# Kernel optimization log

Measured on AMD Instinct MI355X. Metric: run time of the kernel, lower is better.

Reference implementation:

```python
import jax, jax.numpy as jnp
import numpy as np

B, N, E, H = 8, 1024, 768, 12
HD = E // H  # head_dim = 64
EPS = 1e-5


def setup_inputs() -> dict:
    key = jax.random.key(0)
    ks = jax.random.split(key, 3)
    x = jax.random.normal(ks[0], (B, N, E), dtype=jnp.float32)
    # Packed in-projection like torch nn.MultiheadAttention (in_proj_weight [3E, E])
    w_qkv = jax.random.normal(ks[1], (3 * E, E), dtype=jnp.float32) * (1.0 / np.sqrt(E))
    b_qkv = jnp.zeros((3 * E,), dtype=jnp.float32)
    w_out = jax.random.normal(ks[2], (E, E), dtype=jnp.float32) * (1.0 / np.sqrt(E))
    b_out = jnp.zeros((E,), dtype=jnp.float32)
    ln_g = jnp.ones((E,), dtype=jnp.float32)
    ln_b = jnp.zeros((E,), dtype=jnp.float32)
    return {"x": x, "ln_g": ln_g, "ln_b": ln_b, "w_qkv": w_qkv,
            "b_qkv": b_qkv, "w_out": w_out, "b_out": b_out}


def reference(x, ln_g, ln_b, w_qkv, b_qkv, w_out, b_out):
    # LayerNorm over last dim (eps=1e-5, elementwise affine)
    mu = jnp.mean(x, axis=-1, keepdims=True)
    var = jnp.mean(jnp.square(x - mu), axis=-1, keepdims=True)
    xn = (x - mu) * jax.lax.rsqrt(var + EPS) * ln_g + ln_b

    # Packed QKV projection: torch does x @ in_proj_weight.T + in_proj_bias
    qkv = jnp.einsum('bne,fe->bnf', xn, w_qkv) + b_qkv  # [B, N, 3E]
    q, k, v = jnp.split(qkv, 3, axis=-1)
    # Split heads -> [B, H, N, HD]
    q = q.reshape(B, N, H, HD).transpose(0, 2, 1, 3)
    k = k.reshape(B, N, H, HD).transpose(0, 2, 1, 3)
    v = v.reshape(B, N, H, HD).transpose(0, 2, 1, 3)

    scale = 1.0 / np.sqrt(HD)
    scores = jnp.einsum('bhqd,bhkd->bhqk', q * scale, k)  # [B, H, N, N]
    attn = jax.nn.softmax(scores, axis=-1)
    # (attn_dropout=0.0; need_weights=True forces this manual path in torch,
    #  averaged weights attn.mean(axis=1) are computed but not returned here
    #  since return_attention_map defaults to False)
    ctx = jnp.einsum('bhqk,bhkd->bhqd', attn, v)  # [B, H, N, HD]
    ctx = ctx.transpose(0, 2, 1, 3).reshape(B, N, E)

    out = jnp.einsum('bne,fe->bnf', ctx, w_out) + b_out  # out_proj
    return out
```

## Files before the change

### kernel.cpp

```cpp
#include <hip/hip_runtime.h>
#include <hip/hip_bf16.h>
#include <stdint.h>

#define B_ 8
#define N_ 1024
#define E_ 768
#define H_ 12
#define HD_ 64
#define M_ (B_ * N_)

typedef __attribute__((ext_vector_type(8))) short bf8_t;
typedef __attribute__((ext_vector_type(4))) float f4_t;

__device__ __forceinline__ unsigned short f2bf(float f) {
  unsigned u = __builtin_bit_cast(unsigned, f);
  unsigned r = (u + 0x7fffu + ((u >> 16) & 1u)) >> 16;
  return (unsigned short)r;
}

__device__ __forceinline__ unsigned cvt_pk_bf16(float lo, float hi) {
  unsigned r;
  asm("v_cvt_pk_bf16_f32 %0, %1, %2" : "=v"(r) : "v"(lo), "v"(hi));
  return r;
}

__device__ __forceinline__ void load_lds16(const void* g, void* l) {
  __builtin_amdgcn_global_load_lds(
      (__attribute__((address_space(1))) void*)(g),
      (__attribute__((address_space(3))) void*)(l), 16, 0, 0);
}

__device__ __forceinline__ int swz(int row) {
  return ((row ^ (row >> 3)) & 7) << 3;
}

#define F3(a, b, c) fmaxf(fmaxf((a), (b)), (c))

__global__ void k_cast_bf16(const float* __restrict__ in,
                            unsigned short* __restrict__ out, int n4) {
  int i = blockIdx.x * blockDim.x + threadIdx.x;
  if (i < n4) {
    float4 v = ((const float4*)in)[i];
    ushort4 o;
    o.x = f2bf(v.x); o.y = f2bf(v.y); o.z = f2bf(v.z); o.w = f2bf(v.w);
    ((ushort4*)out)[i] = o;
  }
}

__global__ __launch_bounds__(192) void k_ln(const float* __restrict__ x,
                                            const float* __restrict__ g,
                                            const float* __restrict__ bta,
                                            unsigned short* __restrict__ xn) {
  int row = blockIdx.x;
  int t = threadIdx.x;
  float4 v = ((const float4*)(x + (size_t)row * E_))[t];
  float s = v.x + v.y + v.z + v.w;
  float s2 = v.x * v.x + v.y * v.y + v.z * v.z + v.w * v.w;
  for (int off = 32; off; off >>= 1) {
    s += __shfl_xor(s, off, 64);
    s2 += __shfl_xor(s2, off, 64);
  }
  __shared__ float red[6];
  int lane = t & 63, wv = t >> 6;
  if (lane == 0) { red[wv] = s; red[3 + wv] = s2; }
  __syncthreads();
  s = red[0] + red[1] + red[2];
  s2 = red[3] + red[4] + red[5];
  float mu = s * (1.0f / E_);
  float var = s2 * (1.0f / E_) - mu * mu;
  float rstd = rsqrtf(var + 1e-5f);
  float4 gg = ((const float4*)g)[t];
  float4 bb = ((const float4*)bta)[t];
  ushort4 o;
  o.x = f2bf((v.x - mu) * rstd * gg.x + bb.x);
  o.y = f2bf((v.y - mu) * rstd * gg.y + bb.y);
  o.z = f2bf((v.z - mu) * rstd * gg.z + bb.z);
  o.w = f2bf((v.w - mu) * rstd * gg.w + bb.w);
  ((ushort4*)(xn + (size_t)row * E_))[t] = o;
}

template <int EPI>
__global__ __launch_bounds__(256) void k_gemm_bt(
    const unsigned short* __restrict__ A,
    const unsigned short* __restrict__ W,
    const float* __restrict__ bias,
    unsigned short* __restrict__ oQ, unsigned short* __restrict__ oK,
    unsigned short* __restrict__ oVt, float* __restrict__ oF,
    int K, int Nf) {
  __shared__ unsigned short Al[2][128 * 64];
  __shared__ unsigned short Bl[2][128 * 64];
  const int nbx = Nf >> 7;
  const int nwg = nbx << 6;
  const int orig = blockIdx.y * nbx + blockIdx.x;
  const int id = (orig & 7) * (nwg >> 3) + (orig >> 3);
  const int n0 = (id % nbx) * 128, m0 = (id / nbx) * 128;
  const int tid = threadIdx.x;
  const int lane = tid & 63, wv = tid >> 6;
  const int wr = wv >> 1, wc = wv & 1;
  const int g = lane >> 4, l15 = lane & 15;
  f4_t acc[4][4] = {};

  auto stage = [&](int k0, int buf) {
#pragma unroll
    for (int i = 0; i < 4; ++i) {
      int e = (i * 256 + tid) * 8;
      int r = e >> 6;
      int c = (e & 63) ^ swz(r);
      load_lds16(A + (size_t)(m0 + r) * K + (k0 + c), &Al[buf][e]);
      load_lds16(W + (size_t)(n0 + r) * K + (k0 + c), &Bl[buf][e]);
    }
  };

  stage(0, 0);
  __syncthreads();
  int cur = 0;

  for (int k0 = 0; k0 < K; k0 += 64) {
    if (k0 + 64 < K) stage(k0 + 64, cur ^ 1);
    const unsigned short* Ac = Al[cur];
    const unsigned short* Bc = Bl[cur];
#pragma unroll
    for (int kk = 0; kk < 2; ++kk) {
      bf8_t af[4], bfr[4];
#pragma unroll
      for (int mi = 0; mi < 4; ++mi) {
        int ar = wr * 64 + mi * 16 + l15;
        af[mi] = *(const bf8_t*)&Ac[(ar * 64 + kk * 32 + g * 8) ^ swz(ar)];
      }
#pragma unroll
      for (int ni = 0; ni < 4; ++ni) {
        int br = wc * 64 + ni * 16 + l15;
        bfr[ni] = *(const bf8_t*)&Bc[(br * 64 + kk * 32 + g * 8) ^ swz(br)];
      }
#pragma unroll
      for (int mi = 0; mi < 4; ++mi)
#pragma unroll
        for (int ni = 0; ni < 4; ++ni)
          acc[mi][ni] = __builtin_amdgcn_mfma_f32_16x16x32_bf16(
              af[mi], bfr[ni], acc[mi][ni], 0, 0, 0);
    }
    __syncthreads();
    cur ^= 1;
  }

#pragma unroll
  for (int mi = 0; mi < 4; ++mi) {
#pragma unroll
    for (int ni = 0; ni < 4; ++ni) {
      int f = n0 + wc * 64 + ni * 16 + l15;
      float bs = bias[f];
#pragma unroll
      for (int i = 0; i < 4; ++i) {
        int m = m0 + wr * 64 + mi * 16 + g * 4 + i;
        float val = acc[mi][ni][i] + bs;
        if (EPI == 0) {
          int bb = m >> 10, n = m & 1023;
          int which = f / E_;
          int e2 = f - which * E_;
          int h = e2 >> 6, d = e2 & 63;
          size_t qk = (((size_t)bb * H_ + h) * N_ + n) * HD_ + d;
          if (which == 0) oQ[qk] = f2bf(val * 0.1803368801f);
          else if (which == 1) oK[qk] = f2bf(val);
          else oVt[(((size_t)bb * H_ + h) * HD_ + d) * N_ + n] = f2bf(val);
        } else {
          oF[(size_t)m * E_ + f] = val;
        }
      }
    }
  }
}

__global__ __launch_bounds__(256) void k_attn(
    const unsigned short* __restrict__ Q,
    const unsigned short* __restrict__ Kb,
    const unsigned short* __restrict__ Vt,
    unsigned short* __restrict__ ctx) {
  __shared__ unsigned short Kl[2][64 * 64];
  __shared__ unsigned short Vl[2][64 * 64];
  __shared__ unsigned short Pl[4][16 * 64];
  const int bh = blockIdx.x;
  const int qt = blockIdx.y;
  const int tid = threadIdx.x;
  const int lane = tid & 63, wv = tid >> 6;
  const int g = lane >> 4, l15 = lane & 15;

  const unsigned short* Qp = Q + ((size_t)bh * N_ + qt * 64 + wv * 16) * HD_;
  bf8_t qf[2];
#pragma unroll
  for (int kk = 0; kk < 2; ++kk)
    qf[kk] = *(const bf8_t*)&Qp[(size_t)l15 * HD_ + kk * 32 + g * 8];

  f4_t o[4] = {};
  float mrow = -1e30f, lrow = 0.f;
  const unsigned short* Kbase = Kb + (size_t)bh * N_ * HD_;
  const unsigned short* Vbase = Vt + (size_t)bh * HD_ * N_;

  auto stage = [&](int t, int buf) {
#pragma unroll
    for (int i = 0; i < 2; ++i) {
      int e = (i * 256 + tid) * 8;
      int r = e >> 6;
      int c = (e & 63) ^ swz(r);
      load_lds16(Kbase + (size_t)(t * 64 + r) * HD_ + c, &Kl[buf][e]);
      load_lds16(Vbase + (size_t)r * N_ + (t * 64 + c), &Vl[buf][e]);
    }
  };

  stage(0, 0);
  __syncthreads();
  int cur = 0;
  unsigned short* Pw = &Pl[wv][0];

  for (int t = 0; t < 16; ++t) {
    if (t + 1 < 16) stage(t + 1, cur ^ 1);
    const unsigned short* Klc = Kl[cur];
    const unsigned short* Vlc = Vl[cur];

    f4_t s[4] = {};
    __builtin_amdgcn_s_setprio(1);
#pragma unroll
    for (int ni = 0; ni < 4; ++ni) {
      int krow = ni * 16 + l15;
#pragma unroll
      for (int kk = 0; kk < 2; ++kk) {
        bf8_t kf = *(const bf8_t*)&Klc[(krow * 64 + kk * 32 + g * 8) ^ swz(krow)];
        s[ni] = __builtin_amdgcn_mfma_f32_16x16x32_bf16(kf, qf[kk], s[ni], 0, 0, 0);
      }
    }
    __builtin_amdgcn_s_setprio(0);

    float t0 = F3(s[0][0], s[0][1], s[0][2]);
    float t1 = F3(s[0][3], s[1][0], s[1][1]);
    float t2 = F3(s[1][2], s[1][3], s[2][0]);
    float t3 = F3(s[2][1], s[2][2], s[2][3]);
    float t4 = F3(s[3][0], s[3][1], s[3][2]);
    float mx = fmaxf(F3(F3(t0, t1, t2), t3, t4), s[3][3]);
    mx = fmaxf(mx, __shfl_xor(mx, 16, 64));
    mx = fmaxf(mx, __shfl_xor(mx, 32, 64));

    if (!__all(mx - mrow <= 8.0f)) {
      float mnew = fmaxf(mrow, mx);
      float al = exp2f(mrow - mnew);
      lrow *= al;
#pragma unroll
      for (int di = 0; di < 4; ++di)
#pragma unroll
        for (int i = 0; i < 4; ++i) o[di][i] *= al;
      mrow = mnew;
    }

    float r = 0.f;
#pragma unroll
    for (int ni = 0; ni < 4; ++ni)
#pragma unroll
      for (int i = 0; i < 4; ++i) {
        float p = exp2f(s[ni][i] - mrow);
        s[ni][i] = p;
        r += p;
      }
    r += __shfl_xor(r, 16, 64);
    r += __shfl_xor(r, 32, 64);
    lrow += r;

#pragma unroll
    for (int ni = 0; ni < 4; ++ni) {
      uint2 pk;
      pk.x = cvt_pk_bf16(s[ni][0], s[ni][1]);
      pk.y = cvt_pk_bf16(s[ni][2], s[ni][3]);
      int pe = l15 * 64 + ((ni * 16 + g * 4) ^ ((l15 & 7) << 3));
      *(uint2*)&Pw[pe] = pk;
    }
    asm volatile("s_waitcnt lgkmcnt(0)" ::: "memory");
    __builtin_amdgcn_sched_barrier(0);

    __builtin_amdgcn_s_setprio(1);
#pragma unroll
    for (int kk = 0; kk < 2; ++kk) {
      bf8_t pf = *(const bf8_t*)&Pw[l15 * 64 + (((kk * 32 + g * 8)) ^ ((l15 & 7) << 3))];
#pragma unroll
      for (int di = 0; di < 4; ++di) {
        int vrow = di * 16 + l15;
        bf8_t vf = *(const bf8_t*)&Vlc[(vrow * 64 + kk * 32 + g * 8) ^ swz(vrow)];
        o[di] = __builtin_amdgcn_mfma_f32_16x16x32_bf16(vf, pf, o[di], 0, 0, 0);
      }
    }
    __builtin_amdgcn_s_setprio(0);

    __syncthreads();
    cur ^= 1;
  }

  float rinv = 1.0f / lrow;
#pragma unroll
  for (int di = 0; di < 4; ++di) {
    uint2 pk;
    pk.x = cvt_pk_bf16(o[di][0] * rinv, o[di][1] * rinv);
    pk.y = cvt_pk_bf16(o[di][2] * rinv, o[di][3] * rinv);
    int oe = l15 * 64 + ((di * 16 + g * 4) ^ ((l15 & 7) << 3));
    *(uint2*)&Pw[oe] = pk;
  }
  asm volatile("s_waitcnt lgkmcnt(0)" ::: "memory");
  __builtin_amdgcn_sched_barrier(0);

  const int bb = bh / H_, h = bh - bb * H_;
  const int rr = lane >> 2, cb = (lane & 3) * 16;
#pragma unroll
  for (int m2 = 0; m2 < 2; ++m2) {
    int e = rr * 64 + ((cb + 8 * m2) ^ ((rr & 7) << 3));
    bf8_t val = *(const bf8_t*)&Pw[e];
    unsigned short* dst =
        ctx + ((size_t)bb * N_ + qt * 64 + wv * 16 + rr) * E_ + h * HD_ + cb + 8 * m2;
    *(bf8_t*)dst = val;
  }
}

extern "C" void kernel_launch(void* const* d_in, const int* in_sizes, int n_in,
                              void* d_out, int out_size, void* d_ws, size_t ws_size,
                              hipStream_t stream) {
  const float* x     = (const float*)d_in[0];
  const float* ln_g  = (const float*)d_in[1];
  const float* ln_b  = (const float*)d_in[2];
  const float* w_qkv = (const float*)d_in[3];
  const float* b_qkv = (const float*)d_in[4];
  const float* w_out = (const float*)d_in[5];
  const float* b_out = (const float*)d_in[6];
  float* out = (float*)d_out;

  char* ws = (char*)d_ws;
  const size_t SZ = (size_t)M_ * E_ * 2;
  unsigned short* xn    = (unsigned short*)(ws);
  unsigned short* qb    = (unsigned short*)(ws + SZ);
  unsigned short* kbuf  = (unsigned short*)(ws + 2 * SZ);
  unsigned short* vtb   = (unsigned short*)(ws + 3 * SZ);
  unsigned short* ctx   = (unsigned short*)(ws + 4 * SZ);
  unsigned short* wqkvb = (unsigned short*)(ws + 5 * SZ);
  unsigned short* woutb = (unsigned short*)(ws + 5 * SZ + (size_t)3 * E_ * E_ * 2);

  int n1 = 3 * E_ * E_ / 4;
  k_cast_bf16<<<(n1 + 255) / 256, 256, 0, stream>>>(w_qkv, wqkvb, n1);
  int n2 = E_ * E_ / 4;
  k_cast_bf16<<<(n2 + 255) / 256, 256, 0, stream>>>(w_out, woutb, n2);

  k_ln<<<M_, 192, 0, stream>>>(x, ln_g, ln_b, xn);

  k_gemm_bt<0><<<dim3(18, 64), 256, 0, stream>>>(xn, wqkvb, b_qkv, qb, kbuf, vtb,
                                                 nullptr, E_, 3 * E_);
  k_attn<<<dim3(96, 16), 256, 0, stream>>>(qb, kbuf, vtb, ctx);
  k_gemm_bt<1><<<dim3(6, 64), 256, 0, stream>>>(ctx, woutb, b_out, nullptr, nullptr,
                                                nullptr, out, E_, E_);
}
```

Before: 165.6 us.

## Process two query tiles per attention block to reuse K/V tiles

Each attention block now handles 128 query rows, with every wave holding two independent 16-row query fragments that share each staged K/V tile from LDS. The grid is halved along the query dimension, so K/V global traffic and staging per query row drop and MFMA work per LDS read doubles. The per-tile cross-lane row-sum shuffles are deferred to the end, and the max shuffles now run only when the rescale branch fires. This raises register and LDS use per block and halves the number of blocks (768), which may lower occupancy and load balance across CUs.

```diff
diff --git a/kernel.cpp b/kernel.cpp
--- a/kernel.cpp
+++ b/kernel.cpp
@@ -177,21 +177,24 @@
     unsigned short* __restrict__ ctx) {
   __shared__ unsigned short Kl[2][64 * 64];
   __shared__ unsigned short Vl[2][64 * 64];
-  __shared__ unsigned short Pl[4][16 * 64];
+  __shared__ unsigned short Pl[4][2][16 * 64];
   const int bh = blockIdx.x;
   const int qt = blockIdx.y;
   const int tid = threadIdx.x;
   const int lane = tid & 63, wv = tid >> 6;
   const int g = lane >> 4, l15 = lane & 15;
 
-  const unsigned short* Qp = Q + ((size_t)bh * N_ + qt * 64 + wv * 16) * HD_;
-  bf8_t qf[2];
-#pragma unroll
-  for (int kk = 0; kk < 2; ++kk)
-    qf[kk] = *(const bf8_t*)&Qp[(size_t)l15 * HD_ + kk * 32 + g * 8];
-
-  f4_t o[4] = {};
-  float mrow = -1e30f, lrow = 0.f;
+  const unsigned short* Qp = Q + ((size_t)bh * N_ + qt * 128 + wv * 16) * HD_;
+  bf8_t qfa[2], qfb[2];
+#pragma unroll
+  for (int kk = 0; kk < 2; ++kk) {
+    qfa[kk] = *(const bf8_t*)&Qp[(size_t)l15 * HD_ + kk * 32 + g * 8];
+    qfb[kk] = *(const bf8_t*)&Qp[(size_t)(64 + l15) * HD_ + kk * 32 + g * 8];
+  }
+
+  f4_t oa[4] = {}, ob[4] = {};
+  float mra = -1e30f, lra = 0.f;
+  float mrb = -1e30f, lrb = 0.f;
   const unsigned short* Kbase = Kb + (size_t)bh * N_ * HD_;
   const unsigned short* Vbase = Vt + (size_t)bh * HD_ * N_;
 
@@ -209,14 +212,15 @@
   stage(0, 0);
   __syncthreads();
   int cur = 0;
-  unsigned short* Pw = &Pl[wv][0];
+  unsigned short* Pwa = &Pl[wv][0][0];
+  unsigned short* Pwb = &Pl[wv][1][0];
 
   for (int t = 0; t < 16; ++t) {
     if (t + 1 < 16) stage(t + 1, cur ^ 1);
     const unsigned short* Klc = Kl[cur];
     const unsigned short* Vlc = Vl[cur];
 
-    f4_t s[4] = {};
+    f4_t sa[4] = {}, sb[4] = {};
     __builtin_amdgcn_s_setprio(1);
 #pragma unroll
     for (int ni = 0; ni < 4; ++ni) {
@@ -224,51 +228,63 @@
 #pragma unroll
       for (int kk = 0; kk < 2; ++kk) {
         bf8_t kf = *(const bf8_t*)&Klc[(krow * 64 + kk * 32 + g * 8) ^ swz(krow)];
-        s[ni] = __builtin_amdgcn_mfma_f32_16x16x32_bf16(kf, qf[kk], s[ni], 0, 0, 0);
+        sa[ni] = __builtin_amdgcn_mfma_f32_16x16x32_bf16(kf, qfa[kk], sa[ni], 0, 0, 0);
+        sb[ni] = __builtin_amdgcn_mfma_f32_16x16x32_bf16(kf, qfb[kk], sb[ni], 0, 0, 0);
       }
     }
     __builtin_amdgcn_s_setprio(0);
 
-    float t0 = F3(s[0][0], s[0][1], s[0][2]);
-    float t1 = F3(s[0][3], s[1][0], s[1][1]);
-    float t2 = F3(s[1][2], s[1][3], s[2][0]);
-    float t3 = F3(s[2][1], s[2][2], s[2][3]);
-    float t4 = F3(s[3][0], s[3][1], s[3][2]);
-    float mx = fmaxf(F3(F3(t0, t1, t2), t3, t4), s[3][3]);
-    mx = fmaxf(mx, __shfl_xor(mx, 16, 64));
-    mx = fmaxf(mx, __shfl_xor(mx, 32, 64));
-
-    if (!__all(mx - mrow <= 8.0f)) {
-      float mnew = fmaxf(mrow, mx);
-      float al = exp2f(mrow - mnew);
-      lrow *= al;
+    float ta0 = F3(sa[0][0], sa[0][1], sa[0][2]);
+    float ta1 = F3(sa[0][3], sa[1][0], sa[1][1]);
+    float ta2 = F3(sa[1][2], sa[1][3], sa[2][0]);
+    float ta3 = F3(sa[2][1], sa[2][2], sa[2][3]);
+    float ta4 = F3(sa[3][0], sa[3][1], sa[3][2]);
+    float mxa = fmaxf(F3(F3(ta0, ta1, ta2), ta3, ta4), sa[3][3]);
+    float tb0 = F3(sb[0][0], sb[0][1], sb[0][2]);
+    float tb1 = F3(sb[0][3], sb[1][0], sb[1][1]);
+    float tb2 = F3(sb[1][2], sb[1][3], sb[2][0]);
+    float tb3 = F3(sb[2][1], sb[2][2], sb[2][3]);
+    float tb4 = F3(sb[3][0], sb[3][1], sb[3][2]);
+    float mxb = fmaxf(F3(F3(tb0, tb1, tb2), tb3, tb4), sb[3][3]);
+
+    bool ok = (mxa - mra <= 8.0f) && (mxb - mrb <= 8.0f);
+    if (!__all(ok)) {
+      float Ma = fmaxf(mxa, __shfl_xor(mxa, 16, 64));
+      Ma = fmaxf(Ma, __shfl_xor(Ma, 32, 64));
+      float Mb = fmaxf(mxb, __shfl_xor(mxb, 16, 64));
+      Mb = fmaxf(Mb, __shfl_xor(Mb, 32, 64));
+      float mna = fmaxf(mra, Ma), mnb = fmaxf(mrb, Mb);
+      float ala = exp2f(mra - mna), alb = exp2f(mrb - mnb);
+      lra *= ala; lrb *= alb;
 #pragma unroll
       for (int di = 0; di < 4; ++di)
 #pragma unroll
-        for (int i = 0; i < 4; ++i) o[di][i] *= al;
-      mrow = mnew;
-    }
-
-    float r = 0.f;
+        for (int i = 0; i < 4; ++i) { oa[di][i] *= ala; ob[di][i] *= alb; }
+      mra = mna; mrb = mnb;
+    }
+
+    float ra = 0.f, rb = 0.f;
 #pragma unroll
     for (int ni = 0; ni < 4; ++ni)
 #pragma unroll
       for (int i = 0; i < 4; ++i) {
-        float p = exp2f(s[ni][i] - mrow);
-        s[ni][i] = p;
-        r += p;
-      }
-    r += __shfl_xor(r, 16, 64);
-    r += __shfl_xor(r, 32, 64);
-    lrow += r;
+        float pa = exp2f(sa[ni][i] - mra);
+        float pb = exp2f(sb[ni][i] - mrb);
+        sa[ni][i] = pa; sb[ni][i] = pb;
+        ra += pa; rb += pb;
+      }
+    lra += ra; lrb += rb;
 
 #pragma unroll
     for (int ni = 0; ni < 4; ++ni) {
-      uint2 pk;
-      pk.x = cvt_pk_bf16(s[ni][0], s[ni][1]);
-      pk.y = cvt_pk_bf16(s[ni][2], s[ni][3]);
       int pe = l15 * 64 + ((ni * 16 + g * 4) ^ ((l15 & 7) << 3));
-      *(uint2*)&Pw[pe] = pk;
+      uint2 pka, pkb;
+      pka.x = cvt_pk_bf16(sa[ni][0], sa[ni][1]);
+      pka.y = cvt_pk_bf16(sa[ni][2], sa[ni][3]);
+      pkb.x = cvt_pk_bf16(sb[ni][0], sb[ni][1]);
+      pkb.y = cvt_pk_bf16(sb[ni][2], sb[ni][3]);
+      *(uint2*)&Pwa[pe] = pka;
+      *(uint2*)&Pwb[pe] = pkb;
     }
     asm volatile("s_waitcnt lgkmcnt(0)" ::: "memory");
     __builtin_amdgcn_sched_barrier(0);
@@ -276,12 +292,15 @@
     __builtin_amdgcn_s_setprio(1);
 #pragma unroll
     for (int kk = 0; kk < 2; ++kk) {
-      bf8_t pf = *(const bf8_t*)&Pw[l15 * 64 + (((kk * 32 + g * 8)) ^ ((l15 & 7) << 3))];
+      int pe = l15 * 64 + ((kk * 32 + g * 8) ^ ((l15 & 7) << 3));
+      bf8_t pfa = *(const bf8_t*)&Pwa[pe];
+      bf8_t pfb = *(const bf8_t*)&Pwb[pe];
 #pragma unroll
       for (int di = 0; di < 4; ++di) {
         int vrow = di * 16 + l15;
         bf8_t vf = *(const bf8_t*)&Vlc[(vrow * 64 + kk * 32 + g * 8) ^ swz(vrow)];
-        o[di] = __builtin_amdgcn_mfma_f32_16x16x32_bf16(vf, pf, o[di], 0, 0, 0);
+        oa[di] = __builtin_amdgcn_mfma_f32_16x16x32_bf16(vf, pfa, oa[di], 0, 0, 0);
+        ob[di] = __builtin_amdgcn_mfma_f32_16x16x32_bf16(vf, pfb, ob[di], 0, 0, 0);
       }
     }
     __builtin_amdgcn_s_setprio(0);
@@ -290,14 +309,19 @@
     cur ^= 1;
   }
 
-  float rinv = 1.0f / lrow;
+  lra += __shfl_xor(lra, 16, 64); lra += __shfl_xor(lra, 32, 64);
+  lrb += __shfl_xor(lrb, 16, 64); lrb += __shfl_xor(lrb, 32, 64);
+  float rinva = 1.0f / lra, rinvb = 1.0f / lrb;
 #pragma unroll
   for (int di = 0; di < 4; ++di) {
-    uint2 pk;
-    pk.x = cvt_pk_bf16(o[di][0] * rinv, o[di][1] * rinv);
-    pk.y = cvt_pk_bf16(o[di][2] * rinv, o[di][3] * rinv);
     int oe = l15 * 64 + ((di * 16 + g * 4) ^ ((l15 & 7) << 3));
-    *(uint2*)&Pw[oe] = pk;
+    uint2 pka, pkb;
+    pka.x = cvt_pk_bf16(oa[di][0] * rinva, oa[di][1] * rinva);
+    pka.y = cvt_pk_bf16(oa[di][2] * rinva, oa[di][3] * rinva);
+    pkb.x = cvt_pk_bf16(ob[di][0] * rinvb, ob[di][1] * rinvb);
+    pkb.y = cvt_pk_bf16(ob[di][2] * rinvb, ob[di][3] * rinvb);
+    *(uint2*)&Pwa[oe] = pka;
+    *(uint2*)&Pwb[oe] = pkb;
   }
   asm volatile("s_waitcnt lgkmcnt(0)" ::: "memory");
   __builtin_amdgcn_sched_barrier(0);
@@ -307,10 +331,11 @@
 #pragma unroll
   for (int m2 = 0; m2 < 2; ++m2) {
     int e = rr * 64 + ((cb + 8 * m2) ^ ((rr & 7) << 3));
-    bf8_t val = *(const bf8_t*)&Pw[e];
-    unsigned short* dst =
-        ctx + ((size_t)bb * N_ + qt * 64 + wv * 16 + rr) * E_ + h * HD_ + cb + 8 * m2;
-    *(bf8_t*)dst = val;
+    bf8_t va = *(const bf8_t*)&Pwa[e];
+    bf8_t vb = *(const bf8_t*)&Pwb[e];
+    size_t rowa = (size_t)bb * N_ + qt * 128 + wv * 16 + rr;
+    *(bf8_t*)(ctx + rowa * E_ + h * HD_ + cb + 8 * m2) = va;
+    *(bf8_t*)(ctx + (rowa + 64) * E_ + h * HD_ + cb + 8 * m2) = vb;
   }
 }
 
@@ -345,7 +370,7 @@
 
   k_gemm_bt<0><<<dim3(18, 64), 256, 0, stream>>>(xn, wqkvb, b_qkv, qb, kbuf, vtb,
                                                  nullptr, E_, 3 * E_);
-  k_attn<<<dim3(96, 16), 256, 0, stream>>>(qb, kbuf, vtb, ctx);
+  k_attn<<<dim3(96, 8), 256, 0, stream>>>(qb, kbuf, vtb, ctx);
   k_gemm_bt<1><<<dim3(6, 64), 256, 0, stream>>>(ctx, woutb, b_out, nullptr, nullptr,
                                                 nullptr, out, E_, E_);
 }
```

New measurement: 166.1 us. Within noise of the previous version (+0.3%).
